# Kernel tuning notes

Hardware: AMD Instinct MI355X
Metric: run time of the kernel (lower is better)

Reference implementation:

```python
import jax, jax.numpy as jnp
import numpy as np

D_MODEL = 1024
N_HEADS = 16
HEAD_DIM = D_MODEL // N_HEADS
N_EXPERTS = 8
TOP_K = 2
D_FF = 4096
B, T = 4, 1024
EPS = 1e-5


def setup_inputs() -> dict:
    key = jax.random.key(0)
    ks = jax.random.split(key, 12)
    s = lambda fan_in: 1.0 / np.sqrt(fan_in)
    x = jax.random.normal(ks[0], (B, T, D_MODEL), dtype=jnp.float32)
    # additive causal mask (0 on/below diagonal, -inf above)
    mask = jnp.where(jnp.tril(jnp.ones((T, T), dtype=bool)), 0.0, -1e9).astype(jnp.float32)
    return {
        "x": x,
        "mask": mask,
        "ln1_g": jnp.ones((D_MODEL,), jnp.float32),
        "ln1_b": jnp.zeros((D_MODEL,), jnp.float32),
        "w_qkv": jax.random.normal(ks[1], (D_MODEL, 3 * D_MODEL), jnp.float32) * s(D_MODEL),
        "w_proj": jax.random.normal(ks[2], (D_MODEL, D_MODEL), jnp.float32) * s(D_MODEL),
        "b_proj": jnp.zeros((D_MODEL,), jnp.float32),
        "ln2_g": jnp.ones((D_MODEL,), jnp.float32),
        "ln2_b": jnp.zeros((D_MODEL,), jnp.float32),
        "w_router": jax.random.normal(ks[3], (D_MODEL, N_EXPERTS), jnp.float32) * s(D_MODEL),
        "w1": jax.random.normal(ks[4], (N_EXPERTS, D_MODEL, D_FF), jnp.float32) * s(D_MODEL),
        "b1": jnp.zeros((N_EXPERTS, D_FF), jnp.float32),
        "w2": jax.random.normal(ks[5], (N_EXPERTS, D_FF, D_MODEL), jnp.float32) * s(D_FF),
        "b2": jnp.zeros((N_EXPERTS, D_MODEL), jnp.float32),
    }


def _layer_norm(x, g, b):
    mu = jnp.mean(x, axis=-1, keepdims=True)
    var = jnp.var(x, axis=-1, keepdims=True)
    return (x - mu) * jax.lax.rsqrt(var + EPS) * g + b


def _rope(q, k):
    # q, k: [B, H, T, hd]; GPT-NeoX half-split rotary
    t = q.shape[2]
    half = HEAD_DIM // 2
    inv_freq = 1.0 / (10000.0 ** (jnp.arange(0, half, dtype=jnp.float32) / half))
    ang = jnp.arange(t, dtype=jnp.float32)[:, None] * inv_freq[None, :]  # [T, half]
    cos = jnp.concatenate([jnp.cos(ang), jnp.cos(ang)], axis=-1)[None, None]  # [1,1,T,hd]
    sin = jnp.concatenate([jnp.sin(ang), jnp.sin(ang)], axis=-1)[None, None]

    def rot_half(u):
        u1, u2 = jnp.split(u, 2, axis=-1)
        return jnp.concatenate([-u2, u1], axis=-1)

    return q * cos + rot_half(q) * sin, k * cos + rot_half(k) * sin


def _attention(x, mask, w_qkv, w_proj, b_proj):
    b, t, _ = x.shape
    qkv = x @ w_qkv  # [B,T,3D]
    q, k, v = jnp.split(qkv, 3, axis=-1)
    rs = lambda u: u.reshape(b, t, N_HEADS, HEAD_DIM).transpose(0, 2, 1, 3)
    q, k, v = rs(q), rs(k), rs(v)
    q, k = _rope(q, k)
    scale = HEAD_DIM ** -0.5
    scores = jnp.einsum("bhqd,bhkd->bhqk", q, k) * scale + mask
    attn = jax.nn.softmax(scores, axis=-1)
    out = jnp.einsum("bhqk,bhkd->bhqd", attn, v)
    out = out.transpose(0, 2, 1, 3).reshape(b, t, D_MODEL)
    return out @ w_proj + b_proj


def _moe(x, w_router, w1, b1, w2, b2):
    b, t, d = x.shape
    xf = x.reshape(-1, d)  # [N, d]
    logits = xf @ w_router  # [N, E]
    probs = jax.nn.softmax(logits, axis=-1)
    top_v, top_i = jax.lax.top_k(probs, TOP_K)  # [N, k]
    weights = top_v / jnp.sum(top_v, axis=-1, keepdims=True)
    onehot = jax.nn.one_hot(top_i, N_EXPERTS, dtype=xf.dtype)  # [N, k, E]
    gates = jnp.einsum("nk,nke->ne", weights, onehot)  # [N, E]
    # dense grouped-FFN over experts
    h = jax.nn.gelu(jnp.einsum("nd,edf->enf", xf, w1) + b1[:, None, :], approximate=False)
    y = jnp.einsum("enf,efd->end", h, w2) + b2[:, None, :]
    out = jnp.einsum("end,ne->nd", y, gates).reshape(b, t, d)
    # load-balancing aux loss (Switch-style)
    dispatch = jnp.sum(onehot, axis=1)  # [N, E]
    frac = jnp.mean(dispatch, axis=0) / TOP_K
    mean_prob = jnp.mean(probs, axis=0)
    aux = N_EXPERTS * jnp.sum(frac * mean_prob)
    return out, aux


def reference(x, mask, ln1_g, ln1_b, w_qkv, w_proj, b_proj, ln2_g, ln2_b,
              w_router, w1, b1, w2, b2):
    # dropout is identity (eval / p=0)
    x = x + _attention(_layer_norm(x, ln1_g, ln1_b), mask, w_qkv, w_proj, b_proj)
    moe_out, aux = _moe(_layer_norm(x, ln2_g, ln2_b), w_router, w1, b1, w2, b2)
    x = x + moe_out
    return x, aux
```

## Files before the change

### kernel.cpp

```cpp
#include <hip/hip_runtime.h>
#include <math.h>


typedef __bf16 bf16;
typedef __bf16 bf16x8 __attribute__((ext_vector_type(8)));
typedef float  f32x4  __attribute__((ext_vector_type(4)));

#define D_MODEL 1024
#define SEQ     1024
#define NTOK    4096
#define DFF     4096
#define NEXP    8

__device__ __forceinline__ f32x4 mfma16(bf16x8 a, bf16x8 b, f32x4 c) {
  return __builtin_amdgcn_mfma_f32_16x16x32_bf16(a, b, c, 0, 0, 0);
}

__device__ __forceinline__ void async_cp16(void* lds, const void* g) {
  __builtin_amdgcn_global_load_lds(
      (__attribute__((address_space(1))) void*)(void*)g,
      (__attribute__((address_space(3))) void*)lds, 16, 0, 0);
}

template<bool SPLIT>
__device__ __forceinline__ void gemm_core(
    const bf16* __restrict__ Ahi, const bf16* __restrict__ Alo,
    const bf16* __restrict__ Bhi, const bf16* __restrict__ Blo,
    long aOff0, long aOff1, long bOff0, long bOff1,
    int K, bf16* As, bf16* Bs, f32x4 acc[4][4])
{
  const int tid  = threadIdx.x;
  const int lane = tid & 63, w = tid >> 6;
  const int fr   = lane & 15, quad = lane >> 4;
  const int wm   = w >> 1,    wn   = w & 1;
  bf16* AsD0 = As + (w * 16) * 32;
  bf16* AsD1 = As + (64 + w * 16) * 32;
  bf16* BsD0 = Bs + (w * 16) * 32;
  bf16* BsD1 = Bs + (64 + w * 16) * 32;
  const int nph = SPLIT ? 3 : 1;
  for (int ph = 0; ph < nph; ++ph) {
    const bf16* Ap = (ph == 1) ? Alo : Ahi;
    const bf16* Bp = (ph == 2) ? Blo : Bhi;
    for (int k0 = 0; k0 < K; k0 += 32) {
      async_cp16(AsD0, Ap + aOff0 + k0);
      async_cp16(AsD1, Ap + aOff1 + k0);
      async_cp16(BsD0, Bp + bOff0 + k0);
      async_cp16(BsD1, Bp + bOff1 + k0);
      __syncthreads();
      bf16x8 af[4], bfv[4];
#pragma unroll
      for (int mi = 0; mi < 4; ++mi)
        af[mi] = *(const bf16x8*)&As[(wm * 64 + mi * 16 + fr) * 32 + quad * 8];
#pragma unroll
      for (int ni = 0; ni < 4; ++ni)
        bfv[ni] = *(const bf16x8*)&Bs[(wn * 64 + ni * 16 + fr) * 32 + quad * 8];
#pragma unroll
      for (int mi = 0; mi < 4; ++mi)
#pragma unroll
        for (int ni = 0; ni < 4; ++ni)
          acc[mi][ni] = mfma16(af[mi], bfv[ni], acc[mi][ni]);
      __syncthreads();
    }
  }
}

__global__ void k_transpose_cast(const float* __restrict__ in,
                                 bf16* __restrict__ oh, bf16* __restrict__ ol,
                                 int K, int N)
{
  const long zo = (long)blockIdx.z * K * N;
  __shared__ float tile[32][33];
  const int tx = threadIdx.x & 31, ty = threadIdx.x >> 5;
  const int r0 = blockIdx.y * 32, c0 = blockIdx.x * 32;
#pragma unroll
  for (int j = 0; j < 4; ++j)
    tile[ty + 8 * j][tx] = in[zo + (long)(r0 + ty + 8 * j) * N + (c0 + tx)];
  __syncthreads();
#pragma unroll
  for (int j = 0; j < 4; ++j) {
    float v = tile[tx][ty + 8 * j];
    long  o = zo + (long)(c0 + ty + 8 * j) * K + (r0 + tx);
    bf16 hh = (bf16)v;
    oh[o] = hh;
    if (ol) ol[o] = (bf16)(v - (float)hh);
  }
}

__global__ __launch_bounds__(256) void k_layernorm(
    const float* __restrict__ x, const float* __restrict__ g,
    const float* __restrict__ b, bf16* __restrict__ oh, bf16* __restrict__ ol)
{
  const int tok = blockIdx.x, tid = threadIdx.x;
  const float4 v = ((const float4*)(x + (long)tok * D_MODEL))[tid];
  float s  = v.x + v.y + v.z + v.w;
  float s2 = v.x * v.x + v.y * v.y + v.z * v.z + v.w * v.w;
#pragma unroll
  for (int off = 1; off < 64; off <<= 1) {
    s  += __shfl_xor(s, off);
    s2 += __shfl_xor(s2, off);
  }
  __shared__ float red[8];
  if ((tid & 63) == 0) { red[tid >> 6] = s; red[4 + (tid >> 6)] = s2; }
  __syncthreads();
  s  = red[0] + red[1] + red[2] + red[3];
  s2 = red[4] + red[5] + red[6] + red[7];
  const float mu   = s * (1.0f / D_MODEL);
  const float var  = s2 * (1.0f / D_MODEL) - mu * mu;
  const float rstd = 1.0f / sqrtf(var + 1e-5f);
  const float4 gg = ((const float4*)g)[tid];
  const float4 bb = ((const float4*)b)[tid];
  float o0 = (v.x - mu) * rstd * gg.x + bb.x;
  float o1 = (v.y - mu) * rstd * gg.y + bb.y;
  float o2 = (v.z - mu) * rstd * gg.z + bb.z;
  float o3 = (v.w - mu) * rstd * gg.w + bb.w;
  const long base = (long)tok * D_MODEL + tid * 4;
  bf16 h0 = (bf16)o0, h1 = (bf16)o1, h2 = (bf16)o2, h3 = (bf16)o3;
  oh[base + 0] = h0; oh[base + 1] = h1; oh[base + 2] = h2; oh[base + 3] = h3;
  if (ol) {
    ol[base + 0] = (bf16)(o0 - (float)h0);
    ol[base + 1] = (bf16)(o1 - (float)h1);
    ol[base + 2] = (bf16)(o2 - (float)h2);
    ol[base + 3] = (bf16)(o3 - (float)h3);
  }
}

__global__ __launch_bounds__(256, 2) void k_gemm_qkv(
    const bf16* __restrict__ Ah, const bf16* __restrict__ Al,
    const bf16* __restrict__ Bh, const bf16* __restrict__ Bl,
    float* __restrict__ out)
{
  __shared__ __align__(16) bf16 As[128 * 32];
  __shared__ __align__(16) bf16 Bs[128 * 32];
  const int tid = threadIdx.x, lane = tid & 63, w = tid >> 6;
  const int fr = lane & 15, quad = lane >> 4;
  const int wm = w >> 1, wn = w & 1;
  const int m0 = blockIdx.y * 128, n0 = blockIdx.x * 128;
  const int lrow = w * 16 + (lane >> 2), colk = (lane & 3) * 8;
  long aOff0 = (long)(m0 + lrow) * D_MODEL + colk;
  long aOff1 = aOff0 + 64L * D_MODEL;
  long bOff0 = (long)(n0 + lrow) * D_MODEL + colk;
  long bOff1 = bOff0 + 64L * D_MODEL;
  f32x4 acc[4][4];
  f32x4 zv = {0.f, 0.f, 0.f, 0.f};
#pragma unroll
  for (int i = 0; i < 4; ++i)
#pragma unroll
    for (int j = 0; j < 4; ++j) acc[i][j] = zv;
  gemm_core<true>(Ah, Al, Bh, Bl, aOff0, aOff1, bOff0, bOff1, D_MODEL, As, Bs, acc);
#pragma unroll
  for (int mi = 0; mi < 4; ++mi)
#pragma unroll
    for (int ni = 0; ni < 4; ++ni) {
      const int col = n0 + wn * 64 + ni * 16 + fr;
#pragma unroll
      for (int r = 0; r < 4; ++r) {
        const int row = m0 + wm * 64 + mi * 16 + quad * 4 + r;
        out[(long)row * 3072 + col] = acc[mi][ni][r];
      }
    }
}

__global__ __launch_bounds__(256) void k_rope(
    const float* __restrict__ qkv,
    bf16* __restrict__ qh, bf16* __restrict__ ql,
    bf16* __restrict__ kh, bf16* __restrict__ kl,
    bf16* __restrict__ vh, bf16* __restrict__ vl)
{
  const int tok = blockIdx.x;
  const int t = tok & (SEQ - 1), bb = tok >> 10;
  const int tid = threadIdx.x;
  const float ft = (float)t;
  for (int it = tid; it < 512; it += 256) {
    const int hh = it >> 5, i = it & 31;
    const float inv = powf(10000.0f, -(float)i * (1.0f / 32.0f));
    const float ang = ft * inv;
    float sn, cs;
    sincosf(ang, &sn, &cs);
    const long src = (long)tok * 3072 + hh * 64 + i;
    const float q0 = qkv[src], q1 = qkv[src + 32];
    const float k0 = qkv[src + 1024], k1 = qkv[src + 1024 + 32];
    const float qo0 = q0 * cs - q1 * sn, qo1 = q1 * cs + q0 * sn;
    const float ko0 = k0 * cs - k1 * sn, ko1 = k1 * cs + k0 * sn;
    const long dst = ((long)(bb * 16 + hh) * SEQ + t) * 64 + i;
    bf16 x;
    x = (bf16)qo0; qh[dst] = x;      ql[dst] = (bf16)(qo0 - (float)x);
    x = (bf16)qo1; qh[dst + 32] = x; ql[dst + 32] = (bf16)(qo1 - (float)x);
    x = (bf16)ko0; kh[dst] = x;      kl[dst] = (bf16)(ko0 - (float)x);
    x = (bf16)ko1; kh[dst + 32] = x; kl[dst + 32] = (bf16)(ko1 - (float)x);
  }
  for (int it = tid; it < 1024; it += 256) {
    const int hh = it >> 6, d = it & 63;
    const float vv = qkv[(long)tok * 3072 + 2048 + it];
    const long dst = ((long)(bb * 16 + hh) * SEQ + t) * 64 + d;
    bf16 x = (bf16)vv;
    vh[dst] = x; vl[dst] = (bf16)(vv - (float)x);
  }
}

__global__ __launch_bounds__(256, 2) void k_flash(
    const bf16* __restrict__ qh, const bf16* __restrict__ ql,
    const bf16* __restrict__ kh, const bf16* __restrict__ kl,
    const bf16* __restrict__ vh, const bf16* __restrict__ vl,
    bf16* __restrict__ oh, bf16* __restrict__ ol)
{
  const int qt = blockIdx.x, bhid = blockIdx.y;
  const int tid = threadIdx.x, lane = tid & 63, w = tid >> 6;
  const int fr = lane & 15, quad = lane >> 4;
  __shared__ __align__(16) bf16 Qh[64 * 64], Ql[64 * 64];
  __shared__ __align__(16) bf16 Kh[64 * 64], Kl[64 * 64];
  __shared__ __align__(16) bf16 Vh[64 * 64], Vl[64 * 64];
  __shared__ __align__(16) bf16 Ps[4][16 * 64], Pl[4][16 * 64];

  const long qbase = ((long)bhid * SEQ + qt * 64) * 64;
  for (int c = tid; c < 512; c += 256) {
    const int row = c >> 3, c8 = (c & 7) << 3;
    *(uint4*)&Qh[row * 64 + c8] = *(const uint4*)&qh[qbase + row * 64 + c8];
    *(uint4*)&Ql[row * 64 + c8] = *(const uint4*)&ql[qbase + row * 64 + c8];
  }
  __syncthreads();
  bf16x8 aQh[2], aQl[2];
#pragma unroll
  for (int kk = 0; kk < 2; ++kk) {
    aQh[kk] = *(const bf16x8*)&Qh[(w * 16 + fr) * 64 + kk * 32 + quad * 8];
    aQl[kk] = *(const bf16x8*)&Ql[(w * 16 + fr) * 64 + kk * 32 + quad * 8];
  }
  f32x4 o[4];
  f32x4 zv = {0.f, 0.f, 0.f, 0.f};
#pragma unroll
  for (int ct = 0; ct < 4; ++ct) o[ct] = zv;
  float m_r[4], l_r[4];
#pragma unroll
  for (int r = 0; r < 4; ++r) { m_r[r] = -1e30f; l_r[r] = 0.f; }

  for (int kt = 0; kt <= qt; ++kt) {
    __syncthreads();
    const long kbase = ((long)bhid * SEQ + kt * 64) * 64;
    for (int c = tid; c < 512; c += 256) {
      const int row = c >> 3, c8 = (c & 7) << 3;
      *(uint4*)&Kh[row * 64 + c8] = *(const uint4*)&kh[kbase + row * 64 + c8];
      *(uint4*)&Kl[row * 64 + c8] = *(const uint4*)&kl[kbase + row * 64 + c8];
      uint4 uh = *(const uint4*)&vh[kbase + row * 64 + c8];
      uint4 ul = *(const uint4*)&vl[kbase + row * 64 + c8];
      const bf16* vph = (const bf16*)&uh;
      const bf16* vpl = (const bf16*)&ul;
#pragma unroll
      for (int j = 0; j < 8; ++j) {
        Vh[(c8 + j) * 64 + row] = vph[j];
        Vl[(c8 + j) * 64 + row] = vpl[j];
      }
    }
    __syncthreads();

    f32x4 s[4];
#pragma unroll
    for (int nt = 0; nt < 4; ++nt) s[nt] = zv;
#pragma unroll
    for (int nt = 0; nt < 4; ++nt)
#pragma unroll
      for (int kk = 0; kk < 2; ++kk) {
        bf16x8 bh8 = *(const bf16x8*)&Kh[(nt * 16 + fr) * 64 + kk * 32 + quad * 8];
        bf16x8 bl8 = *(const bf16x8*)&Kl[(nt * 16 + fr) * 64 + kk * 32 + quad * 8];
        s[nt] = mfma16(aQh[kk], bh8, s[nt]);
        s[nt] = mfma16(aQl[kk], bh8, s[nt]);
        s[nt] = mfma16(aQh[kk], bl8, s[nt]);
      }
    const int qloc = w * 16 + quad * 4;
#pragma unroll
    for (int nt = 0; nt < 4; ++nt)
#pragma unroll
      for (int r = 0; r < 4; ++r) {
        float sv = s[nt][r] * 0.125f;
        if (kt == qt && (nt * 16 + fr) > (qloc + r)) sv = -1e30f;
        s[nt][r] = sv;
      }
    float al4[4];
#pragma unroll
    for (int r = 0; r < 4; ++r) {
      float m = fmaxf(fmaxf(s[0][r], s[1][r]), fmaxf(s[2][r], s[3][r]));
#pragma unroll
      for (int off = 1; off < 16; off <<= 1) m = fmaxf(m, __shfl_xor(m, off));
      const float mn = fmaxf(m_r[r], m);
      al4[r] = expf(m_r[r] - mn);
      m_r[r] = mn;
    }
    float pmat[4][4], ls4[4];
#pragma unroll
    for (int r = 0; r < 4; ++r) ls4[r] = 0.f;
#pragma unroll
    for (int nt = 0; nt < 4; ++nt)
#pragma unroll
      for (int r = 0; r < 4; ++r) {
        const float p = expf(s[nt][r] - m_r[r]);
        pmat[nt][r] = p;
        ls4[r] += p;
      }
#pragma unroll
    for (int r = 0; r < 4; ++r) {
      float l = ls4[r];
#pragma unroll
      for (int off = 1; off < 16; off <<= 1) l += __shfl_xor(l, off);
      l_r[r] = l_r[r] * al4[r] + l;
      o[0][r] *= al4[r]; o[1][r] *= al4[r]; o[2][r] *= al4[r]; o[3][r] *= al4[r];
    }
#pragma unroll
    for (int nt = 0; nt < 4; ++nt)
#pragma unroll
      for (int r = 0; r < 4; ++r) {
        const float p = pmat[nt][r];
        bf16 hh2 = (bf16)p;
        Ps[w][(quad * 4 + r) * 64 + nt * 16 + fr] = hh2;
        Pl[w][(quad * 4 + r) * 64 + nt * 16 + fr] = (bf16)(p - (float)hh2);
      }
    __syncthreads();
#pragma unroll
    for (int kk = 0; kk < 2; ++kk) {
      bf16x8 aPh = *(const bf16x8*)&Ps[w][fr * 64 + kk * 32 + quad * 8];
      bf16x8 aPl = *(const bf16x8*)&Pl[w][fr * 64 + kk * 32 + quad * 8];
#pragma unroll
      for (int ct = 0; ct < 4; ++ct) {
        bf16x8 bVh = *(const bf16x8*)&Vh[(ct * 16 + fr) * 64 + kk * 32 + quad * 8];
        bf16x8 bVl = *(const bf16x8*)&Vl[(ct * 16 + fr) * 64 + kk * 32 + quad * 8];
        o[ct] = mfma16(aPh, bVh, o[ct]);
        o[ct] = mfma16(aPl, bVh, o[ct]);
        o[ct] = mfma16(aPh, bVl, o[ct]);
      }
    }
  }
  const int b_ = bhid >> 4, h_ = bhid & 15;
#pragma unroll
  for (int ct = 0; ct < 4; ++ct)
#pragma unroll
    for (int r = 0; r < 4; ++r) {
      const int tokn = b_ * SEQ + qt * 64 + w * 16 + quad * 4 + r;
      const int col = h_ * 64 + ct * 16 + fr;
      const float val = o[ct][r] / l_r[r];
      bf16 hh3 = (bf16)val;
      oh[(long)tokn * D_MODEL + col] = hh3;
      ol[(long)tokn * D_MODEL + col] = (bf16)(val - (float)hh3);
    }
}

__global__ __launch_bounds__(256, 2) void k_gemm_proj(
    const bf16* __restrict__ Ah, const bf16* __restrict__ Al,
    const bf16* __restrict__ Bh, const bf16* __restrict__ Bl,
    const float* __restrict__ bproj, const float* __restrict__ xin,
    float* __restrict__ out)
{
  __shared__ __align__(16) bf16 As[128 * 32];
  __shared__ __align__(16) bf16 Bs[128 * 32];
  const int tid = threadIdx.x, lane = tid & 63, w = tid >> 6;
  const int fr = lane & 15, quad = lane >> 4;
  const int wm = w >> 1, wn = w & 1;
  const int m0 = blockIdx.y * 128, n0 = blockIdx.x * 128;
  const int lrow = w * 16 + (lane >> 2), colk = (lane & 3) * 8;
  long aOff0 = (long)(m0 + lrow) * D_MODEL + colk;
  long aOff1 = aOff0 + 64L * D_MODEL;
  long bOff0 = (long)(n0 + lrow) * D_MODEL + colk;
  long bOff1 = bOff0 + 64L * D_MODEL;
  f32x4 acc[4][4];
  f32x4 zv = {0.f, 0.f, 0.f, 0.f};
#pragma unroll
  for (int i = 0; i < 4; ++i)
#pragma unroll
    for (int j = 0; j < 4; ++j) acc[i][j] = zv;
  gemm_core<true>(Ah, Al, Bh, Bl, aOff0, aOff1, bOff0, bOff1, D_MODEL, As, Bs, acc);
#pragma unroll
  for (int mi = 0; mi < 4; ++mi)
#pragma unroll
    for (int ni = 0; ni < 4; ++ni) {
      const int col = n0 + wn * 64 + ni * 16 + fr;
#pragma unroll
      for (int r = 0; r < 4; ++r) {
        const int row = m0 + wm * 64 + mi * 16 + quad * 4 + r;
        out[(long)row * D_MODEL + col] =
            acc[mi][ni][r] + bproj[col] + xin[(long)row * D_MODEL + col];
      }
    }
}

__global__ __launch_bounds__(256) void k_router(
    const float* __restrict__ x1, const float* __restrict__ g,
    const float* __restrict__ b, const float* __restrict__ wr,
    int2* __restrict__ topi, float2* __restrict__ topg,
    float* __restrict__ pbuf)
{
  const int tok = blockIdx.x, tid = threadIdx.x;
  const float4 v = ((const float4*)(x1 + (long)tok * D_MODEL))[tid];
  float s  = v.x + v.y + v.z + v.w;
  float s2 = v.x * v.x + v.y * v.y + v.z * v.z + v.w * v.w;
#pragma unroll
  for (int off = 1; off < 64; off <<= 1) {
    s  += __shfl_xor(s, off);
    s2 += __shfl_xor(s2, off);
  }
  __shared__ float red[8];
  __shared__ float lr[4][8];
  if ((tid & 63) == 0) { red[tid >> 6] = s; red[4 + (tid >> 6)] = s2; }
  __syncthreads();
  s  = red[0] + red[1] + red[2] + red[3];
  s2 = red[4] + red[5] + red[6] + red[7];
  const float mu   = s * (1.0f / D_MODEL);
  const float var  = s2 * (1.0f / D_MODEL) - mu * mu;
  const float rstd = 1.0f / sqrtf(var + 1e-5f);
  const float4 gg = ((const float4*)g)[tid];
  const float4 bb = ((const float4*)b)[tid];
  float n4[4];
  n4[0] = (v.x - mu) * rstd * gg.x + bb.x;
  n4[1] = (v.y - mu) * rstd * gg.y + bb.y;
  n4[2] = (v.z - mu) * rstd * gg.z + bb.z;
  n4[3] = (v.w - mu) * rstd * gg.w + bb.w;
  float part[8];
#pragma unroll
  for (int e = 0; e < 8; ++e) part[e] = 0.f;
  const float* wrow = wr + (long)tid * 4 * 8;
#pragma unroll
  for (int c = 0; c < 4; ++c)
#pragma unroll
    for (int e = 0; e < 8; ++e) part[e] += n4[c] * wrow[c * 8 + e];
#pragma unroll
  for (int off = 1; off < 64; off <<= 1)
#pragma unroll
    for (int e = 0; e < 8; ++e) part[e] += __shfl_xor(part[e], off);
  if ((tid & 63) == 0)
#pragma unroll
    for (int e = 0; e < 8; ++e) lr[tid >> 6][e] = part[e];
  __syncthreads();
  if (tid == 0) {
    float lg[8];
#pragma unroll
    for (int e = 0; e < 8; ++e) lg[e] = lr[0][e] + lr[1][e] + lr[2][e] + lr[3][e];
    float mx = lg[0];
#pragma unroll
    for (int e = 1; e < 8; ++e) mx = fmaxf(mx, lg[e]);
    float pe[8], ssum = 0.f;
#pragma unroll
    for (int e = 0; e < 8; ++e) { pe[e] = expf(lg[e] - mx); ssum += pe[e]; }
    const float inv = 1.0f / ssum;
    int i1 = -1, i2 = -1;
    float v1 = -1.f, v2 = -1.f;
#pragma unroll
    for (int e = 0; e < 8; ++e) {
      const float p = pe[e] * inv;
      pbuf[(long)tok * 8 + e] = p;
      if (p > v1)      { v2 = v1; i2 = i1; v1 = p; i1 = e; }
      else if (p > v2) { v2 = p; i2 = e; }
    }
    const float wsum = v1 + v2;
    topi[tok] = make_int2(i1, i2);
    topg[tok] = make_float2(v1 / wsum, v2 / wsum);
  }
}

__global__ __launch_bounds__(256) void k_scatter(
    const int2* __restrict__ topi, const float2* __restrict__ topg,
    int* __restrict__ ecnt, int* __restrict__ perm, float* __restrict__ gatew)
{
  __shared__ int hcnt[NEXP];
  __shared__ int hbase[NEXP];
  const int tid = threadIdx.x;
  const int tok = blockIdx.x * 256 + tid;
  if (tid < NEXP) hcnt[tid] = 0;
  __syncthreads();
  const int2 ti = topi[tok];
  const float2 tg = topg[tok];
  const int r1 = atomicAdd(&hcnt[ti.x], 1);
  const int r2 = atomicAdd(&hcnt[ti.y], 1);
  __syncthreads();
  if (tid < NEXP) hbase[tid] = atomicAdd(&ecnt[tid], hcnt[tid]);
  __syncthreads();
  const int p1 = hbase[ti.x] + r1;
  perm[ti.x * NTOK + p1] = tok; gatew[ti.x * NTOK + p1] = tg.x;
  const int p2 = hbase[ti.y] + r2;
  perm[ti.y * NTOK + p2] = tok; gatew[ti.y * NTOK + p2] = tg.y;
}

__global__ __launch_bounds__(256) void k_finalize(
    const int* __restrict__ ecnt, const float* __restrict__ pbuf,
    int* __restrict__ eoff, float* __restrict__ aux_out)
{
  __shared__ float partial[256];
  const int tid = threadIdx.x;
  const int e = tid & 7, i0 = tid >> 3;
  float sum = 0.f;
  for (int i = i0; i < NTOK; i += 32) sum += pbuf[(long)i * 8 + e];
  partial[tid] = sum;
  __syncthreads();
  if (tid < 8) {
    float ps = 0.f;
#pragma unroll
    for (int j = 0; j < 32; ++j) ps += partial[j * 8 + tid];
    partial[tid] = ps;
  }
  __syncthreads();
  if (tid == 0) {
    int off = 0;
    float aux = 0.f;
    for (int e2 = 0; e2 < 8; ++e2) {
      eoff[e2] = off;
      off += (ecnt[e2] + 127) & ~127;
      aux += ((float)ecnt[e2] * (1.0f / (NTOK * 2.0f))) * (partial[e2] * (1.0f / NTOK));
    }
    aux_out[0] = 8.0f * aux;
  }
}

__global__ __launch_bounds__(256, 2) void k_gemm_ffn1(
    const bf16* __restrict__ A, const bf16* __restrict__ w1t,
    const float* __restrict__ b1, const int* __restrict__ ecnt,
    const int* __restrict__ eoff, const int* __restrict__ perm,
    bf16* __restrict__ h)
{
  const int e = blockIdx.y >> 5, mt = blockIdx.y & 31;
  const int cnt = ecnt[e];
  if (mt * 128 >= cnt) return;
  __shared__ __align__(16) bf16 As[128 * 32];
  __shared__ __align__(16) bf16 Bs[128 * 32];
  const int tid = threadIdx.x, lane = tid & 63, w = tid >> 6;
  const int fr = lane & 15, quad = lane >> 4;
  const int wm = w >> 1, wn = w & 1;
  const int n0 = blockIdx.x * 128;
  const int lrow = w * 16 + (lane >> 2), colk = (lane & 3) * 8;
  int i0 = mt * 128 + lrow;
  int i1 = i0 + 64;
  i0 = min(i0, cnt - 1);
  i1 = min(i1, cnt - 1);
  const int* pe = perm + e * NTOK;
  long aOff0 = (long)pe[i0] * D_MODEL + colk;
  long aOff1 = (long)pe[i1] * D_MODEL + colk;
  const bf16* B = w1t + (long)e * DFF * D_MODEL;
  long bOff0 = (long)(n0 + lrow) * D_MODEL + colk;
  long bOff1 = bOff0 + 64L * D_MODEL;
  f32x4 acc[4][4];
  f32x4 zv = {0.f, 0.f, 0.f, 0.f};
#pragma unroll
  for (int i = 0; i < 4; ++i)
#pragma unroll
    for (int j = 0; j < 4; ++j) acc[i][j] = zv;
  gemm_core<false>(A, A, B, B, aOff0, aOff1, bOff0, bOff1, D_MODEL, As, Bs, acc);
  const int hbase = eoff[e] + mt * 128;
#pragma unroll
  for (int mi = 0; mi < 4; ++mi)
#pragma unroll
    for (int ni = 0; ni < 4; ++ni) {
      const int col = n0 + wn * 64 + ni * 16 + fr;
#pragma unroll
      for (int r = 0; r < 4; ++r) {
        const int irow = wm * 64 + mi * 16 + quad * 4 + r;
        const float vv = acc[mi][ni][r] + b1[e * DFF + col];
        const float ge = 0.5f * vv * (1.0f + erff(vv * 0.70710678118654752f));
        h[(long)(hbase + irow) * DFF + col] = (bf16)ge;
      }
    }
}

__global__ __launch_bounds__(256, 2) void k_gemm_ffn2(
    const bf16* __restrict__ hbuf, const bf16* __restrict__ w2t,
    const float* __restrict__ b2, const int* __restrict__ ecnt,
    const int* __restrict__ eoff, const int* __restrict__ perm,
    const float* __restrict__ gatew, float* __restrict__ out)
{
  const int e = blockIdx.y >> 5, mt = blockIdx.y & 31;
  const int cnt = ecnt[e];
  if (mt * 128 >= cnt) return;
  __shared__ __align__(16) bf16 As[128 * 32];
  __shared__ __align__(16) bf16 Bs[128 * 32];
  const int tid = threadIdx.x, lane = tid & 63, w = tid >> 6;
  const int fr = lane & 15, quad = lane >> 4;
  const int wm = w >> 1, wn = w & 1;
  const int n0 = blockIdx.x * 128;
  const int lrow = w * 16 + (lane >> 2), colk = (lane & 3) * 8;
  const bf16* A = hbuf + (long)(eoff[e] + mt * 128) * DFF;
  long aOff0 = (long)lrow * DFF + colk;
  long aOff1 = aOff0 + 64L * DFF;
  const bf16* B = w2t + (long)e * D_MODEL * DFF;
  long bOff0 = (long)(n0 + lrow) * DFF + colk;
  long bOff1 = bOff0 + 64L * DFF;
  f32x4 acc[4][4];
  f32x4 zv = {0.f, 0.f, 0.f, 0.f};
#pragma unroll
  for (int i = 0; i < 4; ++i)
#pragma unroll
    for (int j = 0; j < 4; ++j) acc[i][j] = zv;
  gemm_core<false>(A, A, B, B, aOff0, aOff1, bOff0, bOff1, DFF, As, Bs, acc);
#pragma unroll
  for (int mi = 0; mi < 4; ++mi)
#pragma unroll
    for (int ni = 0; ni < 4; ++ni) {
      const int col = n0 + wn * 64 + ni * 16 + fr;
#pragma unroll
      for (int r = 0; r < 4; ++r) {
        const int irow = wm * 64 + mi * 16 + quad * 4 + r;
        const int gi = mt * 128 + irow;
        if (gi < cnt) {
          const int tok = perm[e * NTOK + gi];
          const float gw = gatew[e * NTOK + gi];
          const float vv = acc[mi][ni][r] + b2[e * D_MODEL + col];
          atomicAdd(&out[(long)tok * D_MODEL + col], vv * gw);
        }
      }
    }
}

extern "C" void kernel_launch(void* const* d_in, const int* in_sizes, int n_in,
                              void* d_out, int out_size, void* d_ws, size_t ws_size,
                              hipStream_t stream) {
  const float* x     = (const float*)d_in[0];
  const float* ln1g  = (const float*)d_in[2];
  const float* ln1b  = (const float*)d_in[3];
  const float* wqkv  = (const float*)d_in[4];
  const float* wproj = (const float*)d_in[5];
  const float* bproj = (const float*)d_in[6];
  const float* ln2g  = (const float*)d_in[7];
  const float* ln2b  = (const float*)d_in[8];
  const float* wrout = (const float*)d_in[9];
  const float* w1    = (const float*)d_in[10];
  const float* b1    = (const float*)d_in[11];
  const float* w2    = (const float*)d_in[12];
  const float* b2    = (const float*)d_in[13];
  float* out = (float*)d_out;

  char* p = (char*)d_ws;
  auto alloc = [&](size_t n) { char* r = p; p += (n + 255) & ~(size_t)255; return r; };

  bf16* wqkvT_h = (bf16*)alloc(3072L * 1024 * 2);
  bf16* wqkvT_l = (bf16*)alloc(3072L * 1024 * 2);
  bf16* wprojT_h = (bf16*)alloc(1024L * 1024 * 2);
  bf16* wprojT_l = (bf16*)alloc(1024L * 1024 * 2);
  bf16* w1T = (bf16*)alloc(8L * 4096 * 1024 * 2);
  bf16* w2T = (bf16*)alloc(8L * 1024 * 4096 * 2);
  bf16* ln_h = (bf16*)alloc(4096L * 1024 * 2);
  bf16* ln_l = (bf16*)alloc(4096L * 1024 * 2);
  bf16* attn_h = (bf16*)alloc(4096L * 1024 * 2);
  bf16* attn_l = (bf16*)alloc(4096L * 1024 * 2);
  int*   perm  = (int*)alloc(8L * 4096 * 4);
  float* gatew = (float*)alloc(8L * 4096 * 4);
  int2*  topi  = (int2*)alloc(4096L * 8);
  float2* topg = (float2*)alloc(4096L * 8);
  float* pbuf  = (float*)alloc(4096L * 8 * 4);
  char*  ctrl  = alloc(256);
  int*   ecnt  = (int*)ctrl;
  int*   eoff  = (int*)(ctrl + 64);
  char* big = alloc(100663296);
  float* qkvf = (float*)big;
  bf16* qh = (bf16*)(big + 50331648);
  bf16* ql = qh + 4194304;
  bf16* kh = ql + 4194304;
  bf16* kl = kh + 4194304;
  bf16* vh = kl + 4194304;
  bf16* vl = vh + 4194304;
  bf16* hbuf = (bf16*)big;

  dim3 blk(256);

  k_transpose_cast<<<dim3(3072 / 32, 1024 / 32, 1), blk, 0, stream>>>(wqkv, wqkvT_h, wqkvT_l, 1024, 3072);
  k_transpose_cast<<<dim3(1024 / 32, 1024 / 32, 1), blk, 0, stream>>>(wproj, wprojT_h, wprojT_l, 1024, 1024);
  k_transpose_cast<<<dim3(4096 / 32, 1024 / 32, 8), blk, 0, stream>>>(w1, w1T, nullptr, 1024, 4096);
  k_transpose_cast<<<dim3(1024 / 32, 4096 / 32, 8), blk, 0, stream>>>(w2, w2T, nullptr, 4096, 1024);
  hipMemsetAsync(ctrl, 0, 256, stream);

  k_layernorm<<<4096, blk, 0, stream>>>(x, ln1g, ln1b, ln_h, ln_l);
  k_gemm_qkv<<<dim3(24, 32), blk, 0, stream>>>(ln_h, ln_l, wqkvT_h, wqkvT_l, qkvf);
  k_rope<<<4096, blk, 0, stream>>>(qkvf, qh, ql, kh, kl, vh, vl);
  k_flash<<<dim3(16, 64), blk, 0, stream>>>(qh, ql, kh, kl, vh, vl, attn_h, attn_l);
  k_gemm_proj<<<dim3(8, 32), blk, 0, stream>>>(attn_h, attn_l, wprojT_h, wprojT_l, bproj, x, out);

  k_layernorm<<<4096, blk, 0, stream>>>(out, ln2g, ln2b, ln_h, nullptr);
  k_router<<<4096, blk, 0, stream>>>(out, ln2g, ln2b, wrout, topi, topg, pbuf);
  k_scatter<<<16, blk, 0, stream>>>(topi, topg, ecnt, perm, gatew);
  k_finalize<<<1, blk, 0, stream>>>(ecnt, pbuf, eoff, out + 4194304);
  k_gemm_ffn1<<<dim3(32, 256), blk, 0, stream>>>(ln_h, w1T, b1, ecnt, eoff, perm, hbuf);
  k_gemm_ffn2<<<dim3(8, 256), blk, 0, stream>>>(hbuf, w2T, b2, ecnt, eoff, perm, gatew, out);
}
```

Before: 1.107 ms.

## Swizzle flash-attention LDS tiles and alias P buffers onto Q storage

Applies an XOR swizzle to the Q, K, V and P shared-memory tiles in the flash-attention kernel so the MFMA fragment reads and the transposed V writes hit fewer LDS bank conflicts. The separate P buffers are removed, and P is written into the Q staging area, which is dead once Q fragments are in registers. This cuts LDS per block and the launch bound is raised to 3 blocks per SIMD to improve occupancy. Reusing Q storage relies on the existing barriers, and the higher occupancy target may force register spills.

```diff
diff --git a/kernel.cpp b/kernel.cpp
--- a/kernel.cpp
+++ b/kernel.cpp
@@ -20,6 +20,10 @@
   __builtin_amdgcn_global_load_lds(
       (__attribute__((address_space(1))) void*)(void*)g,
       (__attribute__((address_space(3))) void*)lds, 16, 0, 0);
+}
+
+__device__ __forceinline__ int swz(int row, int col) {
+  return row * 64 + (col ^ (((row ^ (row >> 3)) & 7) << 3));
 }
 
 template<bool SPLIT>
@@ -197,7 +201,7 @@
   }
 }
 
-__global__ __launch_bounds__(256, 2) void k_flash(
+__global__ __launch_bounds__(256, 3) void k_flash(
     const bf16* __restrict__ qh, const bf16* __restrict__ ql,
     const bf16* __restrict__ kh, const bf16* __restrict__ kl,
     const bf16* __restrict__ vh, const bf16* __restrict__ vl,
@@ -206,23 +210,23 @@
   const int qt = blockIdx.x, bhid = blockIdx.y;
   const int tid = threadIdx.x, lane = tid & 63, w = tid >> 6;
   const int fr = lane & 15, quad = lane >> 4;
-  __shared__ __align__(16) bf16 Qh[64 * 64], Ql[64 * 64];
+  __shared__ __align__(16) bf16 QP0[64 * 64];
+  __shared__ __align__(16) bf16 QP1[64 * 64];
   __shared__ __align__(16) bf16 Kh[64 * 64], Kl[64 * 64];
   __shared__ __align__(16) bf16 Vh[64 * 64], Vl[64 * 64];
-  __shared__ __align__(16) bf16 Ps[4][16 * 64], Pl[4][16 * 64];
 
   const long qbase = ((long)bhid * SEQ + qt * 64) * 64;
   for (int c = tid; c < 512; c += 256) {
     const int row = c >> 3, c8 = (c & 7) << 3;
-    *(uint4*)&Qh[row * 64 + c8] = *(const uint4*)&qh[qbase + row * 64 + c8];
-    *(uint4*)&Ql[row * 64 + c8] = *(const uint4*)&ql[qbase + row * 64 + c8];
+    *(uint4*)&QP0[swz(row, c8)] = *(const uint4*)&qh[qbase + row * 64 + c8];
+    *(uint4*)&QP1[swz(row, c8)] = *(const uint4*)&ql[qbase + row * 64 + c8];
   }
   __syncthreads();
   bf16x8 aQh[2], aQl[2];
 #pragma unroll
   for (int kk = 0; kk < 2; ++kk) {
-    aQh[kk] = *(const bf16x8*)&Qh[(w * 16 + fr) * 64 + kk * 32 + quad * 8];
-    aQl[kk] = *(const bf16x8*)&Ql[(w * 16 + fr) * 64 + kk * 32 + quad * 8];
+    aQh[kk] = *(const bf16x8*)&QP0[swz(w * 16 + fr, kk * 32 + quad * 8)];
+    aQl[kk] = *(const bf16x8*)&QP1[swz(w * 16 + fr, kk * 32 + quad * 8)];
   }
   f32x4 o[4];
   f32x4 zv = {0.f, 0.f, 0.f, 0.f};
@@ -237,16 +241,16 @@
     const long kbase = ((long)bhid * SEQ + kt * 64) * 64;
     for (int c = tid; c < 512; c += 256) {
       const int row = c >> 3, c8 = (c & 7) << 3;
-      *(uint4*)&Kh[row * 64 + c8] = *(const uint4*)&kh[kbase + row * 64 + c8];
-      *(uint4*)&Kl[row * 64 + c8] = *(const uint4*)&kl[kbase + row * 64 + c8];
+      *(uint4*)&Kh[swz(row, c8)] = *(const uint4*)&kh[kbase + row * 64 + c8];
+      *(uint4*)&Kl[swz(row, c8)] = *(const uint4*)&kl[kbase + row * 64 + c8];
       uint4 uh = *(const uint4*)&vh[kbase + row * 64 + c8];
       uint4 ul = *(const uint4*)&vl[kbase + row * 64 + c8];
       const bf16* vph = (const bf16*)&uh;
       const bf16* vpl = (const bf16*)&ul;
 #pragma unroll
       for (int j = 0; j < 8; ++j) {
-        Vh[(c8 + j) * 64 + row] = vph[j];
-        Vl[(c8 + j) * 64 + row] = vpl[j];
+        Vh[swz(c8 + j, row)] = vph[j];
+        Vl[swz(c8 + j, row)] = vpl[j];
       }
     }
     __syncthreads();
@@ -258,8 +262,8 @@
     for (int nt = 0; nt < 4; ++nt)
 #pragma unroll
       for (int kk = 0; kk < 2; ++kk) {
-        bf16x8 bh8 = *(const bf16x8*)&Kh[(nt * 16 + fr) * 64 + kk * 32 + quad * 8];
-        bf16x8 bl8 = *(const bf16x8*)&Kl[(nt * 16 + fr) * 64 + kk * 32 + quad * 8];
+        bf16x8 bh8 = *(const bf16x8*)&Kh[swz(nt * 16 + fr, kk * 32 + quad * 8)];
+        bf16x8 bl8 = *(const bf16x8*)&Kl[swz(nt * 16 + fr, kk * 32 + quad * 8)];
         s[nt] = mfma16(aQh[kk], bh8, s[nt]);
         s[nt] = mfma16(aQl[kk], bh8, s[nt]);
         s[nt] = mfma16(aQh[kk], bl8, s[nt]);
@@ -302,24 +306,26 @@
       l_r[r] = l_r[r] * al4[r] + l;
       o[0][r] *= al4[r]; o[1][r] *= al4[r]; o[2][r] *= al4[r]; o[3][r] *= al4[r];
     }
+    bf16* Pw0 = QP0 + w * 1024;
+    bf16* Pw1 = QP1 + w * 1024;
 #pragma unroll
     for (int nt = 0; nt < 4; ++nt)
 #pragma unroll
       for (int r = 0; r < 4; ++r) {
         const float p = pmat[nt][r];
         bf16 hh2 = (bf16)p;
-        Ps[w][(quad * 4 + r) * 64 + nt * 16 + fr] = hh2;
-        Pl[w][(quad * 4 + r) * 64 + nt * 16 + fr] = (bf16)(p - (float)hh2);
+        Pw0[swz(quad * 4 + r, nt * 16 + fr)] = hh2;
+        Pw1[swz(quad * 4 + r, nt * 16 + fr)] = (bf16)(p - (float)hh2);
       }
     __syncthreads();
 #pragma unroll
     for (int kk = 0; kk < 2; ++kk) {
-      bf16x8 aPh = *(const bf16x8*)&Ps[w][fr * 64 + kk * 32 + quad * 8];
-      bf16x8 aPl = *(const bf16x8*)&Pl[w][fr * 64 + kk * 32 + quad * 8];
+      bf16x8 aPh = *(const bf16x8*)&Pw0[swz(fr, kk * 32 + quad * 8)];
+      bf16x8 aPl = *(const bf16x8*)&Pw1[swz(fr, kk * 32 + quad * 8)];
 #pragma unroll
       for (int ct = 0; ct < 4; ++ct) {
-        bf16x8 bVh = *(const bf16x8*)&Vh[(ct * 16 + fr) * 64 + kk * 32 + quad * 8];
-        bf16x8 bVl = *(const bf16x8*)&Vl[(ct * 16 + fr) * 64 + kk * 32 + quad * 8];
+        bf16x8 bVh = *(const bf16x8*)&Vh[swz(ct * 16 + fr, kk * 32 + quad * 8)];
+        bf16x8 bVl = *(const bf16x8*)&Vl[swz(ct * 16 + fr, kk * 32 + quad * 8)];
         o[ct] = mfma16(aPh, bVh, o[ct]);
         o[ct] = mfma16(aPl, bVh, o[ct]);
         o[ct] = mfma16(aPh, bVl, o[ct]);
```

Result: faster. 1.079 ms (-2.5%).
